# Performance work log

Hardware: AMD Instinct MI355X
Metric: run time of the kernel (lower is better)

## Reference

```python
import jax, jax.numpy as jnp
import numpy as np

N_GROUP = 4
TOPK_GROUP = 2
TOP_K = 6
ROUTED_SCALE = 2.0

T, H, E, I = 1024, 1024, 16, 704
SHARED_I = 2 * H  # n_shared_experts * hidden_size


def setup_inputs() -> dict:
    key = jax.random.key(0)
    ks = jax.random.split(key, 10)
    s = 0.02
    return {
        "h": jax.random.normal(ks[0], (T, H), jnp.float32),
        "gate_w": jax.random.normal(ks[1], (E, H), jnp.float32) * s,
        "bias": jax.random.normal(ks[2], (E,), jnp.float32) * 0.1,
        "wg": jax.random.normal(ks[3], (E, H, I), jnp.float32) * s,
        "wu": jax.random.normal(ks[4], (E, H, I), jnp.float32) * s,
        "wd": jax.random.normal(ks[5], (E, I, H), jnp.float32) * s,
        "swg": jax.random.normal(ks[6], (H, SHARED_I), jnp.float32) * s,
        "swu": jax.random.normal(ks[7], (H, SHARED_I), jnp.float32) * s,
        "swd": jax.random.normal(ks[8], (SHARED_I, H), jnp.float32) * s,
    }


def _moe_forward(h, gate_w, bias, wg, wu, wd, swg, swu, swd):
    Tn, Hd = h.shape
    En = gate_w.shape[0]
    per_group = En // N_GROUP

    # shared expert (SwiGLU MLP)
    shared = (jax.nn.silu(h @ swg) * (h @ swu)) @ swd  # [T, H]

    # gate: noaux_tc biased grouped top-k routing (DeepSeek-V3 style)
    logits = h @ gate_w.T                      # [T, E]
    scores = jax.nn.sigmoid(logits)            # [T, E]
    scores_for_choice = scores + bias[None, :]
    grp = scores_for_choice.reshape(Tn, N_GROUP, per_group)
    group_scores = jnp.sum(jax.lax.top_k(grp, 2)[0], axis=-1)   # [T, G] top-2 sum
    _, top_groups = jax.lax.top_k(group_scores, TOPK_GROUP)     # [T, TG]
    gmask = jnp.zeros((Tn, N_GROUP), bool).at[
        jnp.arange(Tn)[:, None], top_groups].set(True)
    emask = jnp.repeat(gmask, per_group, axis=1)                # [T, E]
    masked = jnp.where(emask, scores_for_choice, -jnp.inf)
    _, topk_ids = jax.lax.top_k(masked, TOP_K)                  # [T, K]
    topk_w = jnp.take_along_axis(scores, topk_ids, axis=1)      # weights from unbiased scores
    topk_w = topk_w / jnp.sum(topk_w, axis=-1, keepdims=True)   # norm_topk_prob=True

    # sparse combine weights [T, E]
    cw = jnp.zeros((Tn, En), h.dtype).at[
        jnp.arange(Tn)[:, None], topk_ids].add(topk_w)

    # per-expert SwiGLU MLPs (dense over experts, sparse combine)
    g = jnp.einsum('th,ehi->tei', h, wg)
    u = jnp.einsum('th,ehi->tei', h, wu)
    y = jnp.einsum('tei,eih->teh', jax.nn.silu(g) * u, wd)
    routed = jnp.einsum('te,teh->th', cw, y)

    return routed * ROUTED_SCALE + shared


def reference(h, gate_w, bias, wg, wu, wd, swg, swu, swd):
    return _moe_forward(h, gate_w, bias, wg, wu, wd, swg, swu, swd)
```

## Files before the change

kernel.cpp:

```cpp
#include <hip/hip_runtime.h>
#include <hip/hip_bf16.h>
#include <math.h>

#define TT 1024
#define HH 1024
#define NEXP 16
#define NI 704
#define SI 2048
#define UPMAX 506
#define WDTILES 1408
#define DNSHARED 64
#define DNMAX (DNSHARED + 504)

typedef unsigned short us;
typedef __attribute__((ext_vector_type(8))) __bf16 bf16x8;
typedef __attribute__((ext_vector_type(4))) float f32x4;
typedef __attribute__((ext_vector_type(4))) unsigned short us4;

__device__ __forceinline__ us f2bf(float f) {
  unsigned u = __builtin_bit_cast(unsigned, f);
  u += 0x7fffu + ((u >> 16) & 1u);
  return (us)(u >> 16);
}

__device__ __forceinline__ int ldsOff(int row, int kg) {
  return (row * 4 + (kg ^ ((row >> 1) & 3))) * 16;
}

__device__ __forceinline__ void gl16(const void* g, void* l) {
  __builtin_amdgcn_global_load_lds((const __attribute__((address_space(1))) void*)g,
                                   (__attribute__((address_space(3))) void*)l, 16, 0, 0);
}

__device__ __forceinline__ int chunkMap(int b, int n) {
  int q = n >> 3, r = n & 7;
  int c = b & 7, i = b >> 3;
  int base = (c < r) ? c * (q + 1) : r * (q + 1) + (c - r) * q;
  return base + i;
}

__device__ __forceinline__ void tconv_tile(const float* __restrict__ inz,
                                           us* __restrict__ outz,
                                           int C, int ldo, int r0, int c0,
                                           float (*tile)[65]) {
  int t = threadIdx.x;
  int rr = t >> 4, cc = (t & 15) * 4;
  #pragma unroll
  for (int i = 0; i < 4; ++i) {
    f32x4 v = *reinterpret_cast<const f32x4*>(inz + (size_t)(r0 + rr + i * 16) * C + c0 + cc);
    tile[rr + i*16][cc + 0] = v[0];
    tile[rr + i*16][cc + 1] = v[1];
    tile[rr + i*16][cc + 2] = v[2];
    tile[rr + i*16][cc + 3] = v[3];
  }
  __syncthreads();
  int c = t >> 2, rq = t & 3;
  us o0[8], o1[8];
  #pragma unroll
  for (int j = 0; j < 8; ++j) {
    o0[j] = f2bf(tile[rq * 16 + j][c]);
    o1[j] = f2bf(tile[rq * 16 + 8 + j][c]);
  }
  us* op = outz + (size_t)(c0 + c) * ldo + r0 + rq * 16;
  *reinterpret_cast<us4*>(op)      = *reinterpret_cast<us4*>(&o0[0]);
  *reinterpret_cast<us4*>(op + 4)  = *reinterpret_cast<us4*>(&o0[4]);
  *reinterpret_cast<us4*>(op + 8)  = *reinterpret_cast<us4*>(&o1[0]);
  *reinterpret_cast<us4*>(op + 12) = *reinterpret_cast<us4*>(&o1[4]);
}

__device__ __forceinline__ void tconv512(const float* __restrict__ inz,
                                         us* __restrict__ outz,
                                         int i0, int h0, float (*tile)[129]) {
  int t = threadIdx.x;
  int ir = t >> 3, cg = (t & 7) * 4;
  #pragma unroll
  for (int p = 0; p < 4; ++p) {
    f32x4 v = *reinterpret_cast<const f32x4*>(inz + (size_t)(i0 + ir) * HH + h0 + cg + p * 32);
    tile[ir][cg + p*32 + 0] = v[0];
    tile[ir][cg + p*32 + 1] = v[1];
    tile[ir][cg + p*32 + 2] = v[2];
    tile[ir][cg + p*32 + 3] = v[3];
  }
  __syncthreads();
  int c = t >> 2, rq = t & 3;
  us o[16];
  #pragma unroll
  for (int j = 0; j < 16; ++j) o[j] = f2bf(tile[rq * 16 + j][c]);
  us* op = outz + (size_t)(h0 + c) * NI + i0 + rq * 16;
  *reinterpret_cast<us4*>(op)      = *reinterpret_cast<us4*>(&o[0]);
  *reinterpret_cast<us4*>(op + 4)  = *reinterpret_cast<us4*>(&o[4]);
  *reinterpret_cast<us4*>(op + 8)  = *reinterpret_cast<us4*>(&o[8]);
  *reinterpret_cast<us4*>(op + 12) = *reinterpret_cast<us4*>(&o[12]);
}

__global__ __launch_bounds__(256) void k_prep(
    const float* __restrict__ h, const float* __restrict__ gw,
    const float* __restrict__ bias, float* __restrict__ cw,
    us* __restrict__ hb, unsigned* __restrict__ selpk,
    const float* __restrict__ wg, const float* __restrict__ wu,
    const float* __restrict__ swg, const float* __restrict__ swu,
    us* __restrict__ wgb, us* __restrict__ wub,
    us* __restrict__ swgb, us* __restrict__ swub) {
  __shared__ float tile[64][65];
  __shared__ float lgS[NEXP];
  int b = blockIdx.x;
  int tid = threadIdx.x;
  if (b < 1024) {
    int t = b;
    const float* hr = h + (size_t)t * HH;
    {
      f32x4 v = *reinterpret_cast<const f32x4*>(hr + tid * 4);
      us4 p;
      p[0] = f2bf(v[0]); p[1] = f2bf(v[1]); p[2] = f2bf(v[2]); p[3] = f2bf(v[3]);
      *reinterpret_cast<us4*>(hb + (size_t)t * HH + tid * 4) = p;
    }
    int e = tid >> 4, sub = tid & 15;
    const f32x4* hr4 = reinterpret_cast<const f32x4*>(hr);
    const f32x4* gr4 = reinterpret_cast<const f32x4*>(gw + (size_t)e * HH);
    float acc = 0.f;
    for (int i = sub; i < 256; i += 16) {
      f32x4 a = hr4[i], g = gr4[i];
      acc += a[0]*g[0] + a[1]*g[1] + a[2]*g[2] + a[3]*g[3];
    }
    acc += __shfl_down(acc, 8, 16);
    acc += __shfl_down(acc, 4, 16);
    acc += __shfl_down(acc, 2, 16);
    acc += __shfl_down(acc, 1, 16);
    if (sub == 0) lgS[e] = acc;
    __syncthreads();
    if (tid == 0) {
      float sc[NEXP], s4[NEXP];
      for (int i = 0; i < NEXP; ++i) {
        sc[i] = 1.f / (1.f + expf(-lgS[i]));
        s4[i] = sc[i] + bias[i];
      }
      float gs[4];
      for (int g = 0; g < 4; ++g) {
        float a = s4[4*g], bb = s4[4*g+1], c = s4[4*g+2], d = s4[4*g+3];
        float mx01 = fmaxf(a, bb), mn01 = fminf(a, bb);
        float mx23 = fmaxf(c, d), mn23 = fminf(c, d);
        float top = fmaxf(mx01, mx23);
        float sec = (mx01 >= mx23) ? fmaxf(mn01, mx23) : fmaxf(mn23, mx01);
        gs[g] = top + sec;
      }
      int g1 = 0;
      for (int g = 1; g < 4; ++g) if (gs[g] > gs[g1]) g1 = g;
      int g2 = -1;
      for (int g = 0; g < 4; ++g) { if (g == g1) continue; if (g2 < 0 || gs[g] > gs[g2]) g2 = g; }
      int sel[6];
      bool used[NEXP];
      for (int i = 0; i < NEXP; ++i) used[i] = false;
      float wsum = 0.f;
      for (int it = 0; it < 6; ++it) {
        int best = -1; float bv = 0.f;
        for (int i = 0; i < NEXP; ++i) {
          int grp = i >> 2;
          if ((grp != g1 && grp != g2) || used[i]) continue;
          if (best < 0 || s4[i] > bv) { best = i; bv = s4[i]; }
        }
        used[best] = true;
        sel[it] = best;
        wsum += sc[best];
      }
      float inv = 2.0f / wsum;
      unsigned pk = 0;
      for (int it = 0; it < 6; ++it) {
        pk |= (unsigned)sel[it] << (it * 4);
        cw[(size_t)t * NEXP + sel[it]] = sc[sel[it]] * inv;
      }
      selpk[t] = pk;
    }
    return;
  }
  b -= 1024;
  if (b < 2816) {
    int z = b / 176, r = b % 176;
    tconv_tile(wg + (size_t)z * HH * NI, wgb + (size_t)z * NI * HH,
               NI, HH, (r / 11) * 64, (r % 11) * 64, tile);
    return;
  }
  b -= 2816;
  if (b < 2816) {
    int z = b / 176, r = b % 176;
    tconv_tile(wu + (size_t)z * HH * NI, wub + (size_t)z * NI * HH,
               NI, HH, (r / 11) * 64, (r % 11) * 64, tile);
    return;
  }
  b -= 2816;
  if (b < 512) {
    tconv_tile(swg, swgb, SI, HH, (b >> 5) * 64, (b & 31) * 64, tile);
    return;
  }
  b -= 512;
  {
    tconv_tile(swu, swub, SI, HH, (b >> 5) * 64, (b & 31) * 64, tile);
  }
}

__global__ void k_scan(const unsigned* __restrict__ selpk,
                       int* __restrict__ cnt, int* __restrict__ list,
                       int* __restrict__ wlUp, int* __restrict__ wlDn,
                       int* __restrict__ totals) {
  int t = threadIdx.x;
  int w = t >> 6, l = t & 63;
  unsigned pk = selpk[t];
  unsigned short flags = 0;
  #pragma unroll
  for (int j = 0; j < 6; ++j) flags |= (unsigned short)(1u << ((pk >> (j * 4)) & 15));
  __shared__ int wc[16][16];
  __shared__ int pre[16][16];
  __shared__ int tiles_s[16], upo[16], dno[16], totR[2];
  #pragma unroll
  for (int e = 0; e < 16; ++e) {
    unsigned long long bal = __ballot((flags >> e) & 1);
    if (l == 0) wc[w][e] = __popcll(bal);
  }
  __syncthreads();
  if (t < 16) {
    int s = 0;
    for (int ww = 0; ww < 16; ++ww) { pre[ww][t] = s; s += wc[ww][t]; }
    cnt[t] = s;
    tiles_s[t] = (s + 127) >> 7;
  }
  __syncthreads();
  if (t < 16) {
    int uo = 0, dn = 0;
    for (int e2 = 0; e2 < t; ++e2) { uo += 6 * tiles_s[e2]; dn += 8 * tiles_s[e2]; }
    upo[t] = uo; dno[t] = dn;
    if (t == 15) { totR[0] = uo + 6 * tiles_s[15]; totR[1] = dn + 8 * tiles_s[15]; }
  }
  __syncthreads();
  {
    int te = tiles_s[w];
    for (int i = l; i < 6 * te; i += 64) {
      int nt = i / te, mt = i - nt * te;
      wlUp[upo[w] + i] = ((w * 6 + nt) << 3) | mt;
    }
    for (int i = l; i < 8 * te; i += 64) {
      int nt = i / te, mt = i - nt * te;
      wlDn[dno[w] + i] = ((w * 8 + nt) << 3) | mt;
    }
  }
  if (w == 0) {
    for (int j = l; j < 128; j += 64)
      wlUp[totR[0] + j] = ((96 + (j >> 3)) << 3) | (j & 7);
  }
  if (t == 0) { totals[0] = totR[0] + 128; totals[1] = totR[1]; }
  unsigned long long lmask = (l == 0) ? 0ull : ((~0ull) >> (64 - l));
  #pragma unroll
  for (int e = 0; e < 16; ++e) {
    bool f = (flags >> e) & 1;
    unsigned long long bal = __ballot(f);
    if (f) {
      int rank = __popcll(bal & lmask);
      int j = 0;
      #pragma unroll
      for (int jj = 0; jj < 6; ++jj) j += (((pk >> (jj * 4)) & 15) == (unsigned)e) ? jj : 0;
      list[(e << 10) + pre[w][e] + rank] = (t << 3) | j;
    }
  }
}

__global__ void k_tconvS(const float* __restrict__ swd, us* __restrict__ swdT) {
  __shared__ float tile[64][65];
  int b = blockIdx.x;
  tconv_tile(swd, swdT, HH, SI, (b >> 4) * 64, (b & 15) * 64, tile);
}

__global__ __launch_bounds__(512) void k_upT(
    const us* __restrict__ hb,
    const us* __restrict__ wgb, const us* __restrict__ wub,
    const us* __restrict__ swgb, const us* __restrict__ swub,
    const float* __restrict__ cw, const int* __restrict__ list,
    const int* __restrict__ cnt, const int* __restrict__ wlUp,
    const int* __restrict__ totals,
    us* __restrict__ cact_r, us* __restrict__ cact_s,
    const float* __restrict__ wd, us* __restrict__ wdbT) {
  __shared__ __align__(16) char ldsb[73728];
  int tid = threadIdx.x;
  if ((int)blockIdx.x >= UPMAX) {
    int b = blockIdx.x - UPMAX;
    int z = b / 88, r = b % 88;
    tconv512(wd + (size_t)z * NI * HH, wdbT + (size_t)z * HH * NI,
             (r >> 3) * 64, (r & 7) * 128,
             reinterpret_cast<float(*)[129]>(ldsb));
    return;
  }
  int tot = totals[0];
  if ((int)blockIdx.x >= tot) return;
  int item = wlUp[chunkMap(blockIdx.x, tot)];
  int group = item >> 3, mt = item & 7;
  int t0 = mt * 128;
  bool routed = group < 96;
  int e = 0, n0, cntE = TT;
  const us *bgBase, *buBase;
  if (routed) {
    e = group / 6;
    n0 = (group - e * 6) * 128;
    cntE = cnt[e];
    bgBase = wgb + (size_t)e * NI * HH;
    buBase = wub + (size_t)e * NI * HH;
  } else {
    n0 = (group - 96) * 128;
    bgBase = swgb;
    buBase = swub;
  }
  int w = tid >> 6, l = tid & 63;
  int wm = w >> 2, wn = w & 3;
  int lr = l & 15, lg2 = l >> 4;

  int rowA = tid >> 2;
  int kg = (tid & 3) ^ ((rowA >> 1) & 3);
  int tok = t0 + rowA;
  if (routed) tok = (tok < cntE) ? (list[(e << 10) + tok] >> 3) : 0;
  int bRow = n0 + rowA;
  if (routed && bRow >= NI) bRow = NI - 1;
  const us* aS = hb + (size_t)tok * HH + kg * 8;
  const us* gS = bgBase + (size_t)bRow * HH + kg * 8;
  const us* uS = buBase + (size_t)bRow * HH + kg * 8;

  f32x4 accG[4][2] = {};
  f32x4 accU[4][2] = {};

  int wslot = w * 1024;
  auto stage = [&](char* buf) {
    char* b = buf + wslot;
    gl16(aS, b);
    gl16(gS, b + 8192);
    gl16(uS, b + 16384);
    aS += 32; gS += 32; uS += 32;
  };

  char* bA = ldsb;
  char* bB = ldsb + 24576;
  char* bC = ldsb + 49152;
  stage(bA);
  stage(bB);
  for (int ki = 0; ki < 32; ++ki) {
    if (ki < 30) {
      stage(bC);
      asm volatile("s_waitcnt vmcnt(6)" ::: "memory");
    } else if (ki == 30) {
      asm volatile("s_waitcnt vmcnt(3)" ::: "memory");
    } else {
      asm volatile("s_waitcnt vmcnt(0)" ::: "memory");
    }
    __builtin_amdgcn_s_barrier();
    asm volatile("" ::: "memory");
    bf16x8 af[4], bg[2], bu[2];
    #pragma unroll
    for (int rf = 0; rf < 4; ++rf)
      af[rf] = *reinterpret_cast<const bf16x8*>(bA + ldsOff(wm * 64 + rf * 16 + lr, lg2));
    #pragma unroll
    for (int cf = 0; cf < 2; ++cf) {
      int n = wn * 32 + cf * 16 + lr;
      bg[cf] = *reinterpret_cast<const bf16x8*>(bA + 8192  + ldsOff(n, lg2));
      bu[cf] = *reinterpret_cast<const bf16x8*>(bA + 16384 + ldsOff(n, lg2));
    }
    __builtin_amdgcn_s_setprio(1);
    #pragma unroll
    for (int rf = 0; rf < 4; ++rf)
      #pragma unroll
      for (int cf = 0; cf < 2; ++cf) {
        accG[rf][cf] = __builtin_amdgcn_mfma_f32_16x16x32_bf16(af[rf], bg[cf], accG[rf][cf], 0, 0, 0);
        accU[rf][cf] = __builtin_amdgcn_mfma_f32_16x16x32_bf16(af[rf], bu[cf], accU[rf][cf], 0, 0, 0);
      }
    __builtin_amdgcn_s_setprio(0);
    __builtin_amdgcn_s_barrier();
    asm volatile("" ::: "memory");
    char* tp = bA; bA = bB; bB = bC; bC = tp;
  }
  #pragma unroll
  for (int rf = 0; rf < 4; ++rf)
    #pragma unroll
    for (int cf = 0; cf < 2; ++cf)
      #pragma unroll
      for (int r = 0; r < 4; ++r) {
        int row = wm * 64 + rf * 16 + lg2 * 4 + r;
        int col = wn * 32 + cf * 16 + lr;
        float g = accG[rf][cf][r], u = accU[rf][cf][r];
        float act = g / (1.f + __expf(-g)) * u;
        if (routed) {
          int slot = t0 + row;
          if (slot < cntE && n0 + col < NI) {
            int packed = list[(e << 10) + slot];
            float scl = cw[(size_t)(packed >> 3) * NEXP + e];
            cact_r[((size_t)(e << 10) + slot) * NI + n0 + col] = f2bf(act * scl);
          }
        } else {
          cact_s[(size_t)(t0 + row) * SI + n0 + col] = f2bf(act);
        }
      }
}

__global__ __launch_bounds__(256) void k_down(
    const us* __restrict__ cact_r, const us* __restrict__ cact_s,
    const us* __restrict__ wdbT, const us* __restrict__ swdT,
    const int* __restrict__ list, const int* __restrict__ cnt,
    const int* __restrict__ wlDn, const int* __restrict__ totals,
    us* __restrict__ part, float* __restrict__ out) {
  __shared__ __align__(16) char ldsb[32768];
  int tid = threadIdx.x;
  int b = blockIdx.x;
  bool routed;
  int e = 0, nt, mt, kiter, Ksrc, cntE = TT;
  const us *Ab, *Bb;
  if (b < DNSHARED) {
    routed = false;
    nt = b & 7;
    mt = b >> 3;
    kiter = 64;
    Ksrc = SI;
    Ab = cact_s;
    Bb = swdT;
  } else {
    routed = true;
    int rb = b - DNSHARED;
    int tot = totals[1];
    if (rb >= tot) return;
    int item = wlDn[chunkMap(rb, tot)];
    int group = item >> 3;
    mt = item & 7;
    e = group >> 3; nt = group & 7;
    cntE = cnt[e];
    kiter = NI / 32;
    Ksrc = NI;
    Ab = cact_r + (size_t)e * 1024 * NI;
    Bb = wdbT + (size_t)e * 1024 * NI;
  }
  int t0 = mt * 128;
  int n0 = nt * 128;
  int w = tid >> 6, l = tid & 63;
  int wm = w >> 1, wn = w & 1;
  int lr = l & 15, lg2 = l >> 4;

  int rowA = tid >> 2;
  int kg = (tid & 3) ^ ((rowA >> 1) & 3);
  const us* aS0 = Ab + (size_t)(t0 + rowA) * Ksrc + kg * 8;
  const us* aS1 = Ab + (size_t)(t0 + 64 + rowA) * Ksrc + kg * 8;
  const us* bS0 = Bb + (size_t)(n0 + rowA) * Ksrc + kg * 8;
  const us* bS1 = Bb + (size_t)(n0 + 64 + rowA) * Ksrc + kg * 8;

  f32x4 acc[4][4] = {};

  int wslot = w * 1024;
  auto stage = [&](char* buf) {
    char* bp = buf + wslot;
    gl16(aS0, bp);
    gl16(aS1, bp + 4096);
    gl16(bS0, bp + 8192);
    gl16(bS1, bp + 12288);
    aS0 += 32; aS1 += 32; bS0 += 32; bS1 += 32;
  };

  char* bufR = ldsb;
  char* bufW = ldsb + 16384;
  stage(bufR);
  __syncthreads();
  for (int ki = 0; ki < kiter; ++ki) {
    if (ki + 1 < kiter) stage(bufW);
    bf16x8 af[4], bb[4];
    #pragma unroll
    for (int rf = 0; rf < 4; ++rf)
      af[rf] = *reinterpret_cast<const bf16x8*>(bufR + ldsOff(wm * 64 + rf * 16 + lr, lg2));
    #pragma unroll
    for (int cf = 0; cf < 4; ++cf)
      bb[cf] = *reinterpret_cast<const bf16x8*>(bufR + 8192 + ldsOff(wn * 64 + cf * 16 + lr, lg2));
    #pragma unroll
    for (int rf = 0; rf < 4; ++rf)
      #pragma unroll
      for (int cf = 0; cf < 4; ++cf)
        acc[rf][cf] = __builtin_amdgcn_mfma_f32_16x16x32_bf16(af[rf], bb[cf], acc[rf][cf], 0, 0, 0);
    __syncthreads();
    char* tp = bufR; bufR = bufW; bufW = tp;
  }
  #pragma unroll
  for (int rf = 0; rf < 4; ++rf)
    #pragma unroll
    for (int cf = 0; cf < 4; ++cf)
      #pragma unroll
      for (int r = 0; r < 4; ++r) {
        int row = wm * 64 + rf * 16 + lg2 * 4 + r;
        int col = wn * 64 + cf * 16 + lr;
        if (routed) {
          int slot = t0 + row;
          if (slot < cntE) {
            int packed = list[(e << 10) + slot];
            int t = packed >> 3, j = packed & 7;
            part[((size_t)t * 6 + j) * 1024 + n0 + col] = f2bf(acc[rf][cf][r]);
          }
        } else {
          out[(size_t)(t0 + row) * HH + n0 + col] = acc[rf][cf][r];
        }
      }
}

__global__ void k_reduce(const us* __restrict__ part, float* __restrict__ out) {
  int i = (blockIdx.x * blockDim.x + threadIdx.x) * 4;
  int t = i >> 10, hh = i & 1023;
  f32x4 s = *reinterpret_cast<const f32x4*>(out + i);
  #pragma unroll
  for (int j = 0; j < 6; ++j) {
    us4 p = *reinterpret_cast<const us4*>(part + ((size_t)t * 6 + j) * 1024 + hh);
    #pragma unroll
    for (int k = 0; k < 4; ++k)
      s[k] += __builtin_bit_cast(float, (unsigned)p[k] << 16);
  }
  *reinterpret_cast<f32x4*>(out + i) = s;
}

#define HB_OFF    0ULL
#define CW_OFF    2097152ULL
#define CNT_OFF   2162688ULL
#define SELPK_OFF 2166784ULL
#define LIST_OFF  2170880ULL
#define WLUP_OFF  2236416ULL
#define WLDN_OFF  2244608ULL
#define TOT_OFF   2252800ULL
#define CACTR_OFF 2260992ULL
#define CACTS_OFF 25329664ULL
#define WGB_OFF   29523968ULL
#define WUB_OFF   52592640ULL
#define SWGB_OFF  75661312ULL
#define SWUB_OFF  79855616ULL
#define WDBT_OFF  84049920ULL
#define SWDT_OFF  SWGB_OFF
#define PART_OFF  WGB_OFF

extern "C" void kernel_launch(void* const* d_in, const int* in_sizes, int n_in,
                              void* d_out, int out_size, void* d_ws, size_t ws_size,
                              hipStream_t stream) {
  const float* h    = (const float*)d_in[0];
  const float* gw   = (const float*)d_in[1];
  const float* bias = (const float*)d_in[2];
  const float* wg   = (const float*)d_in[3];
  const float* wu   = (const float*)d_in[4];
  const float* wd   = (const float*)d_in[5];
  const float* swg  = (const float*)d_in[6];
  const float* swu  = (const float*)d_in[7];
  const float* swd  = (const float*)d_in[8];
  float* out = (float*)d_out;

  char* ws = (char*)d_ws;
  us*       hb     = (us*)(ws + HB_OFF);
  float*    cw     = (float*)(ws + CW_OFF);
  int*      cnt    = (int*)(ws + CNT_OFF);
  unsigned* selpk  = (unsigned*)(ws + SELPK_OFF);
  int*      list   = (int*)(ws + LIST_OFF);
  int*      wlUp   = (int*)(ws + WLUP_OFF);
  int*      wlDn   = (int*)(ws + WLDN_OFF);
  int*      totals = (int*)(ws + TOT_OFF);
  us*       cact_r = (us*)(ws + CACTR_OFF);
  us*       cact_s = (us*)(ws + CACTS_OFF);
  us*       wgb    = (us*)(ws + WGB_OFF);
  us*       wub    = (us*)(ws + WUB_OFF);
  us*       swgb   = (us*)(ws + SWGB_OFF);
  us*       swub   = (us*)(ws + SWUB_OFF);
  us*       wdbT   = (us*)(ws + WDBT_OFF);
  us*       swdT   = (us*)(ws + SWDT_OFF);
  us*       part   = (us*)(ws + PART_OFF);

  k_prep<<<7680, 256, 0, stream>>>(h, gw, bias, cw, hb, selpk,
                                   wg, wu, swg, swu, wgb, wub, swgb, swub);
  k_scan<<<1, 1024, 0, stream>>>(selpk, cnt, list, wlUp, wlDn, totals);

  k_upT<<<UPMAX + WDTILES, 512, 0, stream>>>(hb, wgb, wub, swgb, swub, cw, list,
                                             cnt, wlUp, totals, cact_r, cact_s,
                                             wd, wdbT);

  k_tconvS<<<512, 256, 0, stream>>>(swd, swdT);

  k_down<<<DNMAX, 256, 0, stream>>>(cact_r, cact_s, wdbT, swdT, list, cnt,
                                    wlDn, totals, part, out);
  k_reduce<<<1024, 256, 0, stream>>>(part, out);
}
```

Measured before the change: 136.8 us.

## Triple-buffer down-projection LDS staging with explicit vmcnt waits and MFMA priority

The down-projection GEMM kernel moves from double to triple LDS buffering, keeping two k-tiles of global loads in flight. Partial s_waitcnt vmcnt counts and raw s_barrier calls replace __syncthreads, so each wave waits only for the tile it is about to read. s_setprio is raised around the MFMA block so compute waves get issue priority. LDS use rises from 32KB to 48KB per block, which may lower occupancy, and the hand-counted vmcnt values depend on exactly four global loads per stage.

```diff
diff --git a/kernel.cpp b/kernel.cpp
--- a/kernel.cpp
+++ b/kernel.cpp
@@ -399,7 +399,7 @@
     const int* __restrict__ list, const int* __restrict__ cnt,
     const int* __restrict__ wlDn, const int* __restrict__ totals,
     us* __restrict__ part, float* __restrict__ out) {
-  __shared__ __align__(16) char ldsb[32768];
+  __shared__ __align__(16) char ldsb[49152];
   int tid = threadIdx.x;
   int b = blockIdx.x;
   bool routed;
@@ -453,26 +453,39 @@
     aS0 += 32; aS1 += 32; bS0 += 32; bS1 += 32;
   };
 
-  char* bufR = ldsb;
-  char* bufW = ldsb + 16384;
-  stage(bufR);
-  __syncthreads();
+  char* bA = ldsb;
+  char* bB = ldsb + 16384;
+  char* bC = ldsb + 32768;
+  stage(bA);
+  stage(bB);
   for (int ki = 0; ki < kiter; ++ki) {
-    if (ki + 1 < kiter) stage(bufW);
+    if (ki + 2 < kiter) {
+      stage(bC);
+      asm volatile("s_waitcnt vmcnt(8)" ::: "memory");
+    } else if (ki + 2 == kiter) {
+      asm volatile("s_waitcnt vmcnt(4)" ::: "memory");
+    } else {
+      asm volatile("s_waitcnt vmcnt(0)" ::: "memory");
+    }
+    __builtin_amdgcn_s_barrier();
+    asm volatile("" ::: "memory");
     bf16x8 af[4], bb[4];
     #pragma unroll
     for (int rf = 0; rf < 4; ++rf)
-      af[rf] = *reinterpret_cast<const bf16x8*>(bufR + ldsOff(wm * 64 + rf * 16 + lr, lg2));
+      af[rf] = *reinterpret_cast<const bf16x8*>(bA + ldsOff(wm * 64 + rf * 16 + lr, lg2));
     #pragma unroll
     for (int cf = 0; cf < 4; ++cf)
-      bb[cf] = *reinterpret_cast<const bf16x8*>(bufR + 8192 + ldsOff(wn * 64 + cf * 16 + lr, lg2));
+      bb[cf] = *reinterpret_cast<const bf16x8*>(bA + 8192 + ldsOff(wn * 64 + cf * 16 + lr, lg2));
+    __builtin_amdgcn_s_setprio(1);
     #pragma unroll
     for (int rf = 0; rf < 4; ++rf)
       #pragma unroll
       for (int cf = 0; cf < 4; ++cf)
         acc[rf][cf] = __builtin_amdgcn_mfma_f32_16x16x32_bf16(af[rf], bb[cf], acc[rf][cf], 0, 0, 0);
-    __syncthreads();
-    char* tp = bufR; bufR = bufW; bufW = tp;
+    __builtin_amdgcn_s_setprio(0);
+    __builtin_amdgcn_s_barrier();
+    asm volatile("" ::: "memory");
+    char* tp = bA; bA = bB; bB = bC; bC = tp;
   }
   #pragma unroll
   for (int rf = 0; rf < 4; ++rf)
```

Result: faster. 131.4 us (-3.9%).
